# Performance work log

Hardware: AMD Instinct MI355X
Metric: run time of the kernel (lower is better)

## Reference

```python
import jax, jax.numpy as jnp
import numpy as np

BITS = 8
CLIP_RATIO = 1.0
MAX_Q = 2 ** (BITS - 1) - 1  # 127
MIN_Q = -(MAX_Q + 1)         # -128


def setup_inputs() -> dict:
    key = jax.random.key(0)
    k1, k2, k3 = jax.random.split(key, 3)
    B, S, K, N = 4, 4096, 2048, 2048
    x = jax.random.normal(k1, (B, S, K), dtype=jnp.float32)
    # learned int8 weight [out_features, in_features] and per-row scale [out_features, 1]
    weight = jax.random.randint(k2, (N, K), MIN_Q, MAX_Q + 1, dtype=jnp.int32).astype(jnp.int8)
    weight_scale = jax.random.uniform(k3, (N, 1), dtype=jnp.float32, minval=1e-3, maxval=1e-2)
    return {"x": x, "weight": weight, "weight_scale": weight_scale}


def _quantize_sym(x):
    # per-token symmetric int8 quantization over the last dim
    mag = jnp.max(jnp.abs(x), axis=-1, keepdims=True) * CLIP_RATIO  # [B,S,1]
    scale = jnp.where(mag == 0, jnp.ones_like(mag), mag / MAX_Q)
    q = jnp.round(jnp.clip(x / scale, MIN_Q, MAX_Q)).astype(jnp.int8)
    return q, scale


def reference(x, weight, weight_scale):
    a, a_s = _quantize_sym(x)  # a: [B,S,K] int8, a_s: [B,S,1] f32
    res = jnp.einsum(
        'bsk,nk->bsn',
        a.astype(jnp.int32), weight.astype(jnp.int32),
    )  # [B,S,N] int32
    # dequantize: activation scale (per token) * weight scale (per out-channel)
    out = (res.astype(jnp.float32) * a_s * weight_scale.T).astype(x.dtype)
    return out
```

## Files before the change

kernel.cpp:

```cpp
#include <hip/hip_runtime.h>
#include <stdint.h>

#define B_DIM 4
#define S_DIM 4096
#define M_DIM (B_DIM * S_DIM)
#define N_DIM 2048
#define K_DIM 2048

#define BM 128
#define BN 128
#define BK 64

typedef int v4i __attribute__((ext_vector_type(4)));

__global__ __launch_bounds__(256) void pack_w_kernel(const int* __restrict__ w32,
                                                     int8_t* __restrict__ w8) {
    const int i = (blockIdx.x * 256 + threadIdx.x) * 8;
    const int4 a = *reinterpret_cast<const int4*>(w32 + i);
    const int4 b = *reinterpret_cast<const int4*>(w32 + i + 4);
    uint32_t lo = (a.x & 255) | ((a.y & 255) << 8) | ((a.z & 255) << 16) | ((uint32_t)(a.w & 255) << 24);
    uint32_t hi = (b.x & 255) | ((b.y & 255) << 8) | ((b.z & 255) << 16) | ((uint32_t)(b.w & 255) << 24);
    int2 pk;
    pk.x = (int)lo;
    pk.y = (int)hi;
    *reinterpret_cast<int2*>(w8 + i) = pk;
}

__global__ __launch_bounds__(256) void quant_kernel(const float* __restrict__ x,
                                                    int8_t* __restrict__ q,
                                                    float* __restrict__ a_s) {
    const int row = blockIdx.x;
    const int t = threadIdx.x;
    const int lane = t & 63;
    const int wid = t >> 6;

    const float* xr = x + (size_t)row * K_DIM;
    const float4* xv = reinterpret_cast<const float4*>(xr);
    float4 v0 = xv[t * 2 + 0];
    float4 v1 = xv[t * 2 + 1];

    float m = fmaxf(fmaxf(fmaxf(fabsf(v0.x), fabsf(v0.y)), fmaxf(fabsf(v0.z), fabsf(v0.w))),
                    fmaxf(fmaxf(fabsf(v1.x), fabsf(v1.y)), fmaxf(fabsf(v1.z), fabsf(v1.w))));

    #pragma unroll
    for (int off = 32; off > 0; off >>= 1)
        m = fmaxf(m, __shfl_xor(m, off));

    __shared__ float wmax[4];
    if (lane == 0) wmax[wid] = m;
    __syncthreads();
    const float mag = fmaxf(fmaxf(wmax[0], wmax[1]), fmaxf(wmax[2], wmax[3]));

    const float scale = (mag == 0.0f) ? 1.0f : (mag / 127.0f);

    float e[8] = {v0.x, v0.y, v0.z, v0.w, v1.x, v1.y, v1.z, v1.w};
    uint32_t lo = 0, hi = 0;
    #pragma unroll
    for (int j = 0; j < 4; ++j) {
        float d = e[j] / scale;
        d = fminf(fmaxf(d, -128.0f), 127.0f);
        int qi = (int)rintf(d);
        lo |= ((uint32_t)(qi & 255)) << (8 * j);
    }
    #pragma unroll
    for (int j = 0; j < 4; ++j) {
        float d = e[4 + j] / scale;
        d = fminf(fmaxf(d, -128.0f), 127.0f);
        int qi = (int)rintf(d);
        hi |= ((uint32_t)(qi & 255)) << (8 * j);
    }

    int2 pk;
    pk.x = (int)lo;
    pk.y = (int)hi;
    reinterpret_cast<int2*>(q + (size_t)row * K_DIM)[t] = pk;

    if (t == 0) a_s[row] = scale;
}

__global__ __launch_bounds__(256, 2) void gemm_i8_kernel(
    const int8_t* __restrict__ A,
    const int8_t* __restrict__ W,
    const float* __restrict__ a_s,
    const float* __restrict__ w_s,
    float* __restrict__ out)
{
    __shared__ __attribute__((aligned(16))) int8_t As[BM * BK];
    __shared__ __attribute__((aligned(16))) int8_t Bs[BN * BK];

    const int t = threadIdx.x;
    const int lane = t & 63;
    const int wid = t >> 6;
    const int wr = wid >> 1;
    const int wc = wid & 1;

    const int nwg = gridDim.x;
    const int cpx = nwg >> 3;
    const int bid = blockIdx.x;
    const int sbid = (bid & 7) * cpx + (bid >> 3);
    const int ntiles_n = N_DIM / BN;
    const int bm = sbid / ntiles_n;
    const int bn = sbid % ntiles_n;

    const int8_t* aPtr = A + (size_t)(bm * BM) * K_DIM;
    const int8_t* wPtr = W + (size_t)(bn * BN) * K_DIM;

    v4i acc[4][4] = {};

    const int frow = lane & 15;
    const int fchunk = lane >> 4;

    for (int k0 = 0; k0 < K_DIM; k0 += BK) {
        #pragma unroll
        for (int i = 0; i < 2; ++i) {
            const int flat = i * 256 + t;
            const int row = flat >> 2;
            const int chunk = flat & 3;
            __builtin_amdgcn_global_load_lds(
                (const __attribute__((address_space(1))) void*)(aPtr + (size_t)row * K_DIM + k0 + chunk * 16),
                (__attribute__((address_space(3))) void*)(As + flat * 16),
                16, 0, 0);
            __builtin_amdgcn_global_load_lds(
                (const __attribute__((address_space(1))) void*)(wPtr + (size_t)row * K_DIM + k0 + chunk * 16),
                (__attribute__((address_space(3))) void*)(Bs + flat * 16),
                16, 0, 0);
        }
        __syncthreads();

        v4i afrag[4];
        v4i bfrag[4];
        #pragma unroll
        for (int mf = 0; mf < 4; ++mf) {
            const int r = wr * 64 + mf * 16 + frow;
            afrag[mf] = *(const v4i*)(As + r * BK + fchunk * 16);
        }
        #pragma unroll
        for (int nf = 0; nf < 4; ++nf) {
            const int r = wc * 64 + nf * 16 + frow;
            bfrag[nf] = *(const v4i*)(Bs + r * BK + fchunk * 16);
        }
        #pragma unroll
        for (int mf = 0; mf < 4; ++mf)
            #pragma unroll
            for (int nf = 0; nf < 4; ++nf)
                acc[mf][nf] = __builtin_amdgcn_mfma_i32_16x16x64_i8(
                    afrag[mf], bfrag[nf], acc[mf][nf], 0, 0, 0);

        __syncthreads();
    }

    const int row0 = bm * BM + wr * 64;
    const int col0 = bn * BN + wc * 64;
    #pragma unroll
    for (int mf = 0; mf < 4; ++mf) {
        const int rbase = row0 + mf * 16 + (lane >> 4) * 4;
        #pragma unroll
        for (int nf = 0; nf < 4; ++nf) {
            const int c = col0 + nf * 16 + (lane & 15);
            const float ws = w_s[c];
            #pragma unroll
            for (int j = 0; j < 4; ++j) {
                const int r = rbase + j;
                const float o = ((float)acc[mf][nf][j] * a_s[r]) * ws;
                out[(size_t)r * N_DIM + c] = o;
            }
        }
    }
}

extern "C" void kernel_launch(void* const* d_in, const int* in_sizes, int n_in,
                              void* d_out, int out_size, void* d_ws, size_t ws_size,
                              hipStream_t stream) {
    const float* x = (const float*)d_in[0];
    const int* w32 = (const int*)d_in[1];
    const float* wscale = (const float*)d_in[2];
    float* out = (float*)d_out;

    int8_t* q = (int8_t*)d_ws;
    float* a_s = (float*)((char*)d_ws + (size_t)M_DIM * K_DIM);
    int8_t* w8 = (int8_t*)((char*)d_ws + (size_t)M_DIM * K_DIM + (size_t)M_DIM * 4);

    pack_w_kernel<<<(N_DIM * K_DIM) / (256 * 8), 256, 0, stream>>>(w32, w8);
    quant_kernel<<<M_DIM, 256, 0, stream>>>(x, q, a_s);

    const int grid = (M_DIM / BM) * (N_DIM / BN);
    gemm_i8_kernel<<<grid, 256, 0, stream>>>(q, w8, a_s, wscale, out);
}
```

Baseline: 314.8 us.

## Enlarge GEMM tiles to 256x256 with 4-stage LDS pipeline and swizzle

The int8 GEMM moves to 256x256 tiles with 512 threads and a 4-buffer dynamic-LDS ring that prefetches three K-tiles ahead. Waits now use explicit vmcnt counts and a single barrier per iteration instead of two syncthreads. LDS rows are XOR-swizzled to avoid bank conflicts on fragment reads, and MFMA issue priority is raised. The quant kernel also multiplies by a reciprocal instead of dividing, which can shift rounding on some elements. The 128 KB of LDS and larger accumulators per thread may limit occupancy.

```diff
diff --git a/kernel.cpp b/kernel.cpp
--- a/kernel.cpp
+++ b/kernel.cpp
@@ -1,15 +1,18 @@
 #include <hip/hip_runtime.h>
 #include <stdint.h>
 
-#define B_DIM 4
-#define S_DIM 4096
-#define M_DIM (B_DIM * S_DIM)
+#define M_DIM 16384
 #define N_DIM 2048
 #define K_DIM 2048
 
-#define BM 128
-#define BN 128
+#define BM 256
+#define BN 256
 #define BK 64
+#define NT (K_DIM / BK)
+#define TILE_A_BYTES (BM * BK)
+#define TILE_B_BYTES (BN * BK)
+#define BUF_BYTES (TILE_A_BYTES + TILE_B_BYTES)
+#define SMEM_BYTES (4 * BUF_BYTES)
 
 typedef int v4i __attribute__((ext_vector_type(4)));
 
@@ -34,8 +37,7 @@
     const int lane = t & 63;
     const int wid = t >> 6;
 
-    const float* xr = x + (size_t)row * K_DIM;
-    const float4* xv = reinterpret_cast<const float4*>(xr);
+    const float4* xv = reinterpret_cast<const float4*>(x + (size_t)row * K_DIM);
     float4 v0 = xv[t * 2 + 0];
     float4 v1 = xv[t * 2 + 1];
 
@@ -51,20 +53,20 @@
     __syncthreads();
     const float mag = fmaxf(fmaxf(wmax[0], wmax[1]), fmaxf(wmax[2], wmax[3]));
 
-    const float scale = (mag == 0.0f) ? 1.0f : (mag / 127.0f);
+    const float inv = (mag == 0.0f) ? 1.0f : (127.0f / mag);
 
     float e[8] = {v0.x, v0.y, v0.z, v0.w, v1.x, v1.y, v1.z, v1.w};
     uint32_t lo = 0, hi = 0;
     #pragma unroll
     for (int j = 0; j < 4; ++j) {
-        float d = e[j] / scale;
+        float d = e[j] * inv;
         d = fminf(fmaxf(d, -128.0f), 127.0f);
         int qi = (int)rintf(d);
         lo |= ((uint32_t)(qi & 255)) << (8 * j);
     }
     #pragma unroll
     for (int j = 0; j < 4; ++j) {
-        float d = e[4 + j] / scale;
+        float d = e[4 + j] * inv;
         d = fminf(fmaxf(d, -128.0f), 127.0f);
         int qi = (int)rintf(d);
         hi |= ((uint32_t)(qi & 255)) << (8 * j);
@@ -75,84 +77,110 @@
     pk.y = (int)hi;
     reinterpret_cast<int2*>(q + (size_t)row * K_DIM)[t] = pk;
 
-    if (t == 0) a_s[row] = scale;
-}
-
-__global__ __launch_bounds__(256, 2) void gemm_i8_kernel(
+    if (t == 0) a_s[row] = (mag == 0.0f) ? 1.0f : (mag / 127.0f);
+}
+
+__global__ __launch_bounds__(512, 2) void gemm_i8_kernel(
     const int8_t* __restrict__ A,
     const int8_t* __restrict__ W,
     const float* __restrict__ a_s,
     const float* __restrict__ w_s,
     float* __restrict__ out)
 {
-    __shared__ __attribute__((aligned(16))) int8_t As[BM * BK];
-    __shared__ __attribute__((aligned(16))) int8_t Bs[BN * BK];
+    extern __shared__ int8_t smem[];
 
     const int t = threadIdx.x;
     const int lane = t & 63;
     const int wid = t >> 6;
-    const int wr = wid >> 1;
-    const int wc = wid & 1;
-
-    const int nwg = gridDim.x;
-    const int cpx = nwg >> 3;
+    const int wr = wid >> 2;
+    const int wc = wid & 3;
+
     const int bid = blockIdx.x;
-    const int sbid = (bid & 7) * cpx + (bid >> 3);
-    const int ntiles_n = N_DIM / BN;
-    const int bm = sbid / ntiles_n;
-    const int bn = sbid % ntiles_n;
-
-    const int8_t* aPtr = A + (size_t)(bm * BM) * K_DIM;
-    const int8_t* wPtr = W + (size_t)(bn * BN) * K_DIM;
-
-    v4i acc[4][4] = {};
+    const int sbid = (bid & 7) * (gridDim.x >> 3) + (bid >> 3);
+    const int bm = sbid >> 3;
+    const int bn = sbid & 7;
+
+    const int8_t* aSrc = A + (size_t)(bm * BM) * K_DIM;
+    const int8_t* bSrc = W + (size_t)(bn * BN) * K_DIM;
+
+    const int f0 = t, f1 = t + 512;
+    const int r0 = f0 >> 2, u0 = f0 & 3;
+    const int r1 = f1 >> 2, u1 = f1 & 3;
+    const size_t gOff0 = (size_t)r0 * K_DIM + (size_t)((u0 ^ ((r0 >> 1) & 3)) << 4);
+    const size_t gOff1 = (size_t)r1 * K_DIM + (size_t)((u1 ^ ((r1 >> 1) & 3)) << 4);
+
+    #define STAGE(tile)                                                                     \
+    do {                                                                                    \
+        int8_t* base_ = smem + ((tile) & 3) * BUF_BYTES;                                    \
+        const int k0_ = (tile) * BK;                                                        \
+        __builtin_amdgcn_global_load_lds(                                                   \
+            (const __attribute__((address_space(1))) void*)(aSrc + k0_ + gOff0),            \
+            (__attribute__((address_space(3))) void*)(base_ + f0 * 16), 16, 0, 0);          \
+        __builtin_amdgcn_global_load_lds(                                                   \
+            (const __attribute__((address_space(1))) void*)(aSrc + k0_ + gOff1),            \
+            (__attribute__((address_space(3))) void*)(base_ + f1 * 16), 16, 0, 0);          \
+        __builtin_amdgcn_global_load_lds(                                                   \
+            (const __attribute__((address_space(1))) void*)(bSrc + k0_ + gOff0),            \
+            (__attribute__((address_space(3))) void*)(base_ + TILE_A_BYTES + f0 * 16), 16, 0, 0); \
+        __builtin_amdgcn_global_load_lds(                                                   \
+            (const __attribute__((address_space(1))) void*)(bSrc + k0_ + gOff1),            \
+            (__attribute__((address_space(3))) void*)(base_ + TILE_A_BYTES + f1 * 16), 16, 0, 0); \
+    } while (0)
 
     const int frow = lane & 15;
-    const int fchunk = lane >> 4;
-
-    for (int k0 = 0; k0 < K_DIM; k0 += BK) {
-        #pragma unroll
-        for (int i = 0; i < 2; ++i) {
-            const int flat = i * 256 + t;
-            const int row = flat >> 2;
-            const int chunk = flat & 3;
-            __builtin_amdgcn_global_load_lds(
-                (const __attribute__((address_space(1))) void*)(aPtr + (size_t)row * K_DIM + k0 + chunk * 16),
-                (__attribute__((address_space(3))) void*)(As + flat * 16),
-                16, 0, 0);
-            __builtin_amdgcn_global_load_lds(
-                (const __attribute__((address_space(1))) void*)(wPtr + (size_t)row * K_DIM + k0 + chunk * 16),
-                (__attribute__((address_space(3))) void*)(Bs + flat * 16),
-                16, 0, 0);
-        }
-        __syncthreads();
-
-        v4i afrag[4];
-        v4i bfrag[4];
-        #pragma unroll
-        for (int mf = 0; mf < 4; ++mf) {
-            const int r = wr * 64 + mf * 16 + frow;
-            afrag[mf] = *(const v4i*)(As + r * BK + fchunk * 16);
-        }
-        #pragma unroll
-        for (int nf = 0; nf < 4; ++nf) {
-            const int r = wc * 64 + nf * 16 + frow;
-            bfrag[nf] = *(const v4i*)(Bs + r * BK + fchunk * 16);
-        }
-        #pragma unroll
-        for (int mf = 0; mf < 4; ++mf)
+    const int fc = lane >> 4;
+    const int rA = wr * 128 + frow;
+    const int rB = wc * 64 + frow;
+    const int aOff = rA * 64 + ((((rA >> 1) & 3) ^ fc) << 4);
+    const int bOff = rB * 64 + ((((rB >> 1) & 3) ^ fc) << 4);
+
+    v4i acc[8][4] = {};
+
+    STAGE(0);
+    STAGE(1);
+    STAGE(2);
+    asm volatile("s_waitcnt vmcnt(8)" ::: "memory");
+    __builtin_amdgcn_s_barrier();
+    asm volatile("" ::: "memory");
+
+    for (int tt = 0; tt < NT; ++tt) {
+        if (tt + 3 < NT) STAGE(tt + 3);
+
+        const int8_t* Ab = smem + (tt & 3) * BUF_BYTES;
+        const int8_t* Bb = Ab + TILE_A_BYTES;
+
+        v4i af[8], bf[4];
+        #pragma unroll
+        for (int mf = 0; mf < 8; ++mf)
+            af[mf] = *(const v4i*)(Ab + aOff + mf * 1024);
+        #pragma unroll
+        for (int nf = 0; nf < 4; ++nf)
+            bf[nf] = *(const v4i*)(Bb + bOff + nf * 1024);
+
+        __builtin_amdgcn_s_setprio(1);
+        #pragma unroll
+        for (int mf = 0; mf < 8; ++mf)
             #pragma unroll
             for (int nf = 0; nf < 4; ++nf)
                 acc[mf][nf] = __builtin_amdgcn_mfma_i32_16x16x64_i8(
-                    afrag[mf], bfrag[nf], acc[mf][nf], 0, 0, 0);
-
-        __syncthreads();
-    }
-
-    const int row0 = bm * BM + wr * 64;
+                    af[mf], bf[nf], acc[mf][nf], 0, 0, 0);
+        __builtin_amdgcn_s_setprio(0);
+
+        if (tt < NT - 1) {
+            asm volatile("" ::: "memory");
+            if (tt < NT - 3)        asm volatile("s_waitcnt vmcnt(8)" ::: "memory");
+            else if (tt < NT - 2)   asm volatile("s_waitcnt vmcnt(4)" ::: "memory");
+            else                    asm volatile("s_waitcnt vmcnt(0)" ::: "memory");
+            __builtin_amdgcn_s_barrier();
+            asm volatile("" ::: "memory");
+        }
+    }
+    #undef STAGE
+
+    const int row0 = bm * BM + wr * 128;
     const int col0 = bn * BN + wc * 64;
     #pragma unroll
-    for (int mf = 0; mf < 4; ++mf) {
+    for (int mf = 0; mf < 8; ++mf) {
         const int rbase = row0 + mf * 16 + (lane >> 4) * 4;
         #pragma unroll
         for (int nf = 0; nf < 4; ++nf) {
@@ -161,8 +189,7 @@
             #pragma unroll
             for (int j = 0; j < 4; ++j) {
                 const int r = rbase + j;
-                const float o = ((float)acc[mf][nf][j] * a_s[r]) * ws;
-                out[(size_t)r * N_DIM + c] = o;
+                out[(size_t)r * N_DIM + c] = ((float)acc[mf][nf][j] * a_s[r]) * ws;
             }
         }
     }
@@ -180,9 +207,16 @@
     float* a_s = (float*)((char*)d_ws + (size_t)M_DIM * K_DIM);
     int8_t* w8 = (int8_t*)((char*)d_ws + (size_t)M_DIM * K_DIM + (size_t)M_DIM * 4);
 
+    static int smem_set = 0;
+    if (!smem_set) {
+        hipFuncSetAttribute(reinterpret_cast<const void*>(&gemm_i8_kernel),
+                            hipFuncAttributeMaxDynamicSharedMemorySize, SMEM_BYTES);
+        smem_set = 1;
+    }
+
     pack_w_kernel<<<(N_DIM * K_DIM) / (256 * 8), 256, 0, stream>>>(w32, w8);
     quant_kernel<<<M_DIM, 256, 0, stream>>>(x, q, a_s);
 
     const int grid = (M_DIM / BM) * (N_DIM / BN);
-    gemm_i8_kernel<<<grid, 256, 0, stream>>>(q, w8, a_s, wscale, out);
-}
+    gemm_i8_kernel<<<grid, 512, SMEM_BYTES, stream>>>(q, w8, a_s, wscale, out);
+}
```

Result: no change. 309.0 us (-1.8%).
